# Optimization experiments

Hardware: AMD Instinct MI355X
Metric: run time of the kernel (lower is better)

## Reference

```python
import jax, jax.numpy as jnp
import numpy as np

B, S, MSL, MQL = 512, 20, 32, 16
E, H, HQ = 32, 32, 32
V, A = 10000, 1000
D = H + S  # per-object feature dim (hidden + one-hot tag) = 52
G = 256


def _lstm_last_h(x, Wih, Whh, bih, bhh):
    # x: [N, T, E]; torch LSTM gate order i,f,g,o; returns final hidden [N, H]
    n, t, _ = x.shape
    h_dim = Whh.shape[1]
    xp = jnp.einsum('nte,ge->ntg', x, Wih) + bih + bhh  # precompute input projection

    def step(carry, xt):
        h, c = carry
        gates = xt + h @ Whh.T
        i, f, g, o = jnp.split(gates, 4, axis=-1)
        c = jax.nn.sigmoid(f) * c + jax.nn.sigmoid(i) * jnp.tanh(g)
        h = jax.nn.sigmoid(o) * jnp.tanh(c)
        return (h, c), None

    init = (jnp.zeros((n, h_dim), x.dtype), jnp.zeros((n, h_dim), x.dtype))
    (h, _), _ = jax.lax.scan(step, init, xp.transpose(1, 0, 2))
    return h


def setup_inputs() -> dict:
    key = jax.random.key(0)
    ks = jax.random.split(key, 24)
    nrm = lambda k, shp, std=0.1: (jax.random.normal(k, shp) * std).astype(jnp.float32)
    inp = {
        'story': jax.random.randint(ks[0], (B, S, MSL), 0, V),
        'question': jax.random.randint(ks[1], (B, MQL), 0, V),
        'emb': nrm(ks[2], (V, E)),
        's_Wih': nrm(ks[3], (4 * H, E)),
        's_Whh': nrm(ks[4], (4 * H, H)),
        's_bih': jnp.zeros((4 * H,), jnp.float32),
        's_bhh': jnp.zeros((4 * H,), jnp.float32),
        'q_Wih': nrm(ks[5], (4 * HQ, E)),
        'q_Whh': nrm(ks[6], (4 * HQ, HQ)),
        'q_bih': jnp.zeros((4 * HQ,), jnp.float32),
        'q_bhh': jnp.zeros((4 * HQ,), jnp.float32),
        'g1_w': nrm(ks[7], (G, 2 * D + HQ)), 'g1_b': jnp.zeros((G,), jnp.float32),
        'g2_w': nrm(ks[8], (G, G)), 'g2_b': jnp.zeros((G,), jnp.float32),
        'g3_w': nrm(ks[9], (G, G)), 'g3_b': jnp.zeros((G,), jnp.float32),
        'g4_w': nrm(ks[10], (G, G)), 'g4_b': jnp.zeros((G,), jnp.float32),
        'f1_w': nrm(ks[11], (G, G)), 'f1_b': jnp.zeros((G,), jnp.float32),
        'f2_w': nrm(ks[12], (512, G)), 'f2_b': jnp.zeros((512,), jnp.float32),
        'f3_w': nrm(ks[13], (A, 512)), 'f3_b': jnp.zeros((A,), jnp.float32),
    }
    return inp


def reference(story, question, emb, s_Wih, s_Whh, s_bih, s_bhh,
              q_Wih, q_Whh, q_bih, q_bhh,
              g1_w, g1_b, g2_w, g2_b, g3_w, g3_b, g4_w, g4_b,
              f1_w, f1_b, f2_w, f2_b, f3_w, f3_b):
    bsz = story.shape[0]
    # story encoding: LSTM over each sentence, take final hidden state
    s_emb = emb[story].reshape(bsz * S, MSL, E)
    s_state = _lstm_last_h(s_emb, s_Wih, s_Whh, s_bih, s_bhh).reshape(bsz, S, H)
    # append one-hot position tags -> story objects [B, S, H+S]
    tags = jnp.broadcast_to(jnp.eye(S, dtype=s_state.dtype), (bsz, S, S))
    obj = jnp.concatenate([s_state, tags], axis=2)
    # question encoding
    q_state = _lstm_last_h(emb[question], q_Wih, q_Whh, q_bih, q_bhh)  # [B, HQ]
    # g_theta over all S*S pairs: g1(cat(o_i, o_j, q)) split into three projections
    Wa, Wb, Wq = g1_w[:, :D], g1_w[:, D:2 * D], g1_w[:, 2 * D:]
    pi = jnp.einsum('bsd,gd->bsg', obj, Wa)   # object-as-first projection
    pj = jnp.einsum('bsd,gd->bsg', obj, Wb)   # object-as-second projection
    pq = q_state @ Wq.T                        # [B, G]
    x = jax.nn.relu(pi[:, :, None, :] + pj[:, None, :, :] + pq[:, None, None, :] + g1_b)  # [B,S,S,G]
    x = jax.nn.relu(jnp.einsum('bijg,hg->bijh', x, g2_w) + g2_b)
    x = jax.nn.relu(jnp.einsum('bijg,hg->bijh', x, g3_w) + g3_b)
    x = jax.nn.relu(jnp.einsum('bijg,hg->bijh', x, g4_w) + g4_b)
    sum_g = x.sum(axis=(1, 2))  # [B, G]
    out = jax.nn.relu(sum_g @ f1_w.T + f1_b)
    out = jax.nn.relu(out @ f2_w.T + f2_b)
    return out @ f3_w.T + f3_b
```

## Files before the change

kernel.cpp:

```cpp
#include <hip/hip_runtime.h>

typedef unsigned short u16;
typedef unsigned int   u32;
typedef __attribute__((ext_vector_type(8))) short short8;
typedef __attribute__((ext_vector_type(4))) float f32x4;

#define OFF_XPS   0
#define OFF_XPQ   1280000
#define OFF_QST   2560000
#define OFF_PI    2576384
#define OFF_PJ    5197824
#define OFF_QA    7819264
#define OFF_TGA   7950336
#define OFF_TGB   7955456
#define OFF_WB    7960576
#define OFF_STB   8058880
#define OFF_WAB   8222720
#define OFF_WBB   8226816
#define OFF_WHHS  8230912
#define OFF_WHHQ  8232960
#define OFF_WF1   8235008
#define OFF_WF2   8267776
#define OFF_WF3   8333312
#define OFF_SGP   0
#define OFF_ACT1  720896
#define OFF_ACT2  786432

__device__ __forceinline__ u16 f2bf(float f){
  union { float f; u32 u; } v; v.f = f;
  u32 u = v.u;
  u32 r = u + 0x7fffu + ((u >> 16) & 1u);
  return (u16)(r >> 16);
}
__device__ __forceinline__ u32 pack2(float a, float b){
  u32 r;
  asm("v_cvt_pk_bf16_f32 %0, %1, %2" : "=v"(r) : "v"(a), "v"(b));
  return r;
}
__device__ __forceinline__ float sigm(float x){
  return __builtin_amdgcn_rcpf(1.f + __expf(-x));
}

#define LBAR() do {                                        \
    asm volatile("s_waitcnt lgkmcnt(0)" ::: "memory");     \
    __builtin_amdgcn_s_barrier();                          \
    __builtin_amdgcn_sched_barrier(0);                     \
  } while (0)

__global__ __launch_bounds__(256) void prep_kernel(
    const float* __restrict__ emb,
    const float* __restrict__ swih, const float* __restrict__ sbih, const float* __restrict__ sbhh,
    const float* __restrict__ qwih, const float* __restrict__ qbih, const float* __restrict__ qbhh,
    const float* __restrict__ g2w, const float* __restrict__ g3w, const float* __restrict__ g4w,
    const float* __restrict__ g1w,
    const float* __restrict__ swhh, const float* __restrict__ qwhh,
    const float* __restrict__ f1w, const float* __restrict__ f2w, const float* __restrict__ f3w,
    float* __restrict__ xps, float* __restrict__ xpq,
    u16* __restrict__ wb, u16* __restrict__ wab, u16* __restrict__ wbb,
    float* __restrict__ tga, float* __restrict__ tgb,
    u16* __restrict__ whhbs, u16* __restrict__ whhbq,
    u16* __restrict__ wf1, u16* __restrict__ wf2, u16* __restrict__ wf3)
{
  __shared__ float wl[4096];
  __shared__ float bl[128];
  const int tid = threadIdx.x;
  if (blockIdx.y == 2){
    const int B = 196608;
    const int C = B + 16384;
    const int D = C + 10240;
    const int E = D + 8192;
    const int F = E + 65536;
    const int G = F + 131072;
    const int H = G + 524288;
    for (int idx = blockIdx.x*256 + tid; idx < H; idx += 160*256){
      if (idx < B){
        const int k = idx;
        const float* src = (k < 65536) ? g2w : ((k < 131072) ? g3w : g4w);
        wb[k] = f2bf(src[k & 65535]);
      } else if (idx < C){
        const int k = idx - B;
        if (k < 8192) wab[k] = f2bf(g1w[(k>>5)*136 + (k&31)]);
        else { const int k2 = k - 8192; wbb[k2] = f2bf(g1w[(k2>>5)*136 + 52 + (k2&31)]); }
      } else if (idx < D){
        const int k = idx - C;
        if (k < 5120){ const int s = k >> 8, g = k & 255; tga[k] = g1w[g*136 + 32 + s]; }
        else { const int k2 = k - 5120; const int s = k2 >> 8, g = k2 & 255; tgb[k2] = g1w[g*136 + 84 + s]; }
      } else if (idx < E){
        const int k = idx - D;
        if (k < 4096) whhbs[k] = f2bf(swhh[k]);
        else whhbq[k-4096] = f2bf(qwhh[k-4096]);
      } else if (idx < F){
        const int k = idx - E;
        wf1[k] = f2bf(f1w[k]);
      } else if (idx < G){
        const int k = idx - F;
        wf2[k] = f2bf(f2w[k]);
      } else {
        const int k = idx - G;
        const int o = k >> 9, kk = k & 511;
        wf3[k] = (o < 1000) ? f2bf(f3w[o*512 + kk]) : (u16)0;
      }
    }
    return;
  }
  const bool isq = blockIdx.y;
  const float* wih = isq ? qwih : swih;
  const float* bih = isq ? qbih : sbih;
  const float* bhh = isq ? qbhh : sbhh;
  float* xp = isq ? xpq : xps;
  #pragma unroll
  for (int k=0;k<16;k++) wl[k*256+tid] = wih[k*256+tid];
  if (tid < 128) bl[tid] = bih[tid] + bhh[tid];
  __syncthreads();
  const int v = blockIdx.x*256 + tid;
  if (v >= 10000) return;
  float4 e[8];
  #pragma unroll
  for (int q=0;q<8;q++) e[q] = *(const float4*)(emb + v*32 + q*4);
  for (int g=0; g<128; ++g){
    float acc = bl[g];
    #pragma unroll
    for (int q=0;q<8;q++){
      float4 w4 = *(const float4*)(&wl[g*32 + q*4]);
      acc = fmaf(e[q].x, w4.x, acc); acc = fmaf(e[q].y, w4.y, acc);
      acc = fmaf(e[q].z, w4.z, acc); acc = fmaf(e[q].w, w4.w, acc);
    }
    xp[v*128 + (g&15)*8 + (g>>4)] = acc;
  }
}

template<int LEN>
__device__ __forceinline__ void lstm_mfma_run(
    const int* __restrict__ toks, int s0,
    const float* __restrict__ xpr, const u16* __restrict__ whhb,
    u16* __restrict__ hl, int lane, float* h0r, float* h1r)
{
  const int l15 = lane & 15, l4 = lane >> 4;
  short8 wf[8];
  #pragma unroll
  for (int f=0; f<8; f++)
    wf[f] = *(const short8*)(whhb + (f*16+l15)*32 + l4*8);
  short8 ha = (short8){0,0,0,0,0,0,0,0};
  float c0[4] = {0,0,0,0}, c1[4] = {0,0,0,0};
  int tk[4];
  #pragma unroll
  for (int r=0;r<4;r++) tk[r] = toks[(s0 + l4*4 + r)*LEN];
  float4 xa[4], xb[4];
  #pragma unroll
  for (int r=0;r<4;r++){
    xa[r] = *(const float4*)(xpr + tk[r]*128 + l15*8);
    xb[r] = *(const float4*)(xpr + tk[r]*128 + l15*8 + 4);
  }
  #pragma unroll
  for (int t=0; t<LEN; ++t){
    int tkn[4];
    if (t+1 < LEN){
      #pragma unroll
      for (int r=0;r<4;r++) tkn[r] = toks[(s0 + l4*4 + r)*LEN + t + 1];
    }
    const f32x4 z = (f32x4){0.f,0.f,0.f,0.f};
    f32x4 acc[8];
    #pragma unroll
    for (int f=0; f<8; f++)
      acc[f] = __builtin_amdgcn_mfma_f32_16x16x32_bf16(ha, wf[f], z, 0, 0, 0);
    float4 na[4], nb[4];
    if (t+1 < LEN){
      #pragma unroll
      for (int r=0;r<4;r++){
        na[r] = *(const float4*)(xpr + tkn[r]*128 + l15*8);
        nb[r] = *(const float4*)(xpr + tkn[r]*128 + l15*8 + 4);
      }
    }
    #pragma unroll
    for (int r=0;r<4;r++){
      float i0 = sigm(acc[0][r] + xa[r].x);
      float f0 = sigm(acc[2][r] + xa[r].z);
      float g0 = 2.f*sigm(2.f*(acc[4][r] + xb[r].x)) - 1.f;
      float o0 = sigm(acc[6][r] + xb[r].z);
      c0[r] = fmaf(f0, c0[r], i0*g0);
      h0r[r] = o0 * (2.f*sigm(2.f*c0[r]) - 1.f);
      float i1 = sigm(acc[1][r] + xa[r].y);
      float f1v = sigm(acc[3][r] + xa[r].w);
      float g1v = 2.f*sigm(2.f*(acc[5][r] + xb[r].y)) - 1.f;
      float o1 = sigm(acc[7][r] + xb[r].w);
      c1[r] = fmaf(f1v, c1[r], i1*g1v);
      h1r[r] = o1 * (2.f*sigm(2.f*c1[r]) - 1.f);
    }
    if (t+1 < LEN){
      #pragma unroll
      for (int r=0;r<4;r++){
        hl[(l4*4+r)*32 + l15]      = f2bf(h0r[r]);
        hl[(l4*4+r)*32 + 16 + l15] = f2bf(h1r[r]);
      }
      __syncthreads();
      ha = *(const short8*)(hl + l15*32 + l4*8);
      #pragma unroll
      for (int r=0;r<4;r++){ xa[r] = na[r]; xb[r] = nb[r]; }
    }
  }
}

__global__ __launch_bounds__(64) void lstm_kernel(
    const int* __restrict__ story, const int* __restrict__ question,
    const float* __restrict__ xprs, const float* __restrict__ xprq,
    const u16* __restrict__ whhbs, const u16* __restrict__ whhbq,
    u16* __restrict__ stb, float* __restrict__ qst)
{
  __shared__ u16 hl[512];
  const int lane = threadIdx.x;
  const int w = blockIdx.x;
  const int l15 = lane & 15, l4 = lane >> 4;
  float h0r[4], h1r[4];
  if (w >= 640){
    const int s0 = (w - 640)*16;
    lstm_mfma_run<16>(question, s0, xprq, whhbq, hl, lane, h0r, h1r);
    #pragma unroll
    for (int r=0;r<4;r++){
      qst[(s0 + l4*4 + r)*32 + l15]      = h0r[r];
      qst[(s0 + l4*4 + r)*32 + 16 + l15] = h1r[r];
    }
  } else {
    const int s0 = w*16;
    lstm_mfma_run<32>(story, s0, xprs, whhbs, hl, lane, h0r, h1r);
    #pragma unroll
    for (int r=0;r<4;r++){
      stb[(s0 + l4*4 + r)*32 + l15]      = f2bf(h0r[r]);
      stb[(s0 + l4*4 + r)*32 + 16 + l15] = f2bf(h1r[r]);
    }
  }
}

__global__ __launch_bounds__(256) void pipj_kernel(
    const u16* __restrict__ stb, const u16* __restrict__ wab, const u16* __restrict__ wbb,
    const float* __restrict__ tga, const float* __restrict__ tgb,
    const float* __restrict__ qst, const float* __restrict__ g1w, const float* __restrict__ g1b,
    float* __restrict__ pi, float* __restrict__ pj, float* __restrict__ qa)
{
  const int tid = threadIdx.x;
  if (blockIdx.y == 2){
    for (int idx = blockIdx.x*256 + tid; idx < 131072; idx += 160*256){
      const int b = idx >> 8, g = idx & 255;
      const float* qs = qst + b*32;
      const float* wr = g1w + g*136 + 104;
      float acc = g1b[g];
      #pragma unroll
      for (int q=0;q<8;q++){
        float4 s4 = *(const float4*)(qs + q*4);
        float4 w4 = *(const float4*)(wr + q*4);
        acc = fmaf(s4.x, w4.x, acc); acc = fmaf(s4.y, w4.y, acc);
        acc = fmaf(s4.z, w4.z, acc); acc = fmaf(s4.w, w4.w, acc);
      }
      qa[idx] = acc;
    }
    return;
  }
  const int lane = tid & 63;
  const int wv = tid >> 6;
  const int l15 = lane & 15;
  const int l4r = lane >> 4;
  const int bs0 = blockIdx.x * 64;
  const bool isj = blockIdx.y;
  const u16* wB = isj ? wbb : wab;
  const float* tg = isj ? tgb : tga;
  float* out = isj ? pj : pi;

  short8 af[4], bf[4];
  #pragma unroll
  for (int mf=0; mf<4; mf++)
    af[mf] = *(const short8*)(stb + (bs0 + mf*16 + l15)*32 + l4r*8);
  #pragma unroll
  for (int nf=0; nf<4; nf++)
    bf[nf] = *(const short8*)(wB + (wv*64 + nf*16 + l15)*32 + l4r*8);

  #pragma unroll
  for (int mf=0; mf<4; mf++){
    #pragma unroll
    for (int nf=0; nf<4; nf++){
      f32x4 acc = (f32x4){0.f,0.f,0.f,0.f};
      acc = __builtin_amdgcn_mfma_f32_16x16x32_bf16(af[mf], bf[nf], acc, 0, 0, 0);
      const int g = wv*64 + nf*16 + l15;
      #pragma unroll
      for (int r=0; r<4; r++){
        const int bs = bs0 + mf*16 + l4r*4 + r;
        const int s = bs % 20;
        out[bs*256 + g] = acc[r] + tg[s*256 + g];
      }
    }
  }
}

#define LDX 264
__global__ __launch_bounds__(512) void relnet_kernel(
    const float* __restrict__ pi, const float* __restrict__ pj, const float* __restrict__ qa,
    const u16* __restrict__ w2, const u16* __restrict__ w3, const u16* __restrict__ w4,
    const float* __restrict__ b2, const float* __restrict__ b3, const float* __restrict__ b4,
    float* __restrict__ sgp)
{
  __shared__ u16 Xs[80*LDX + 6656];
  const int tid = threadIdx.x;
  const int lane = tid & 63;
  const int wv  = tid >> 6;
  const int b   = blockIdx.x;
  const int t   = blockIdx.y;
  const int l15 = lane & 15;
  const int l4  = lane >> 4;

  const float* pib = pi + b*(20*256);
  const float* pjb = pj + b*(20*256);
  const float* qab = qa + b*256;

  const int ar0 = (wv*32 + l15)*256 + l4*8;
  const int ar1 = (wv*32 + 16 + l15)*256 + l4*8;

  #pragma unroll
  for (int it = 0; it < 5; ++it){
    int u  = it*512 + tid;
    int m  = u >> 5;
    int gq = (u & 31) << 3;
    int R  = t*80 + m;
    int i  = R / 20;
    int j  = R - i*20;
    const float4* pr = (const float4*)(pib + i*256 + gq);
    const float4* qr = (const float4*)(pjb + j*256 + gq);
    const float4* ar = (const float4*)(qab + gq);
    uint4 pk;
    {
      float4 a = pr[0], c4 = qr[0], d4 = ar[0];
      pk.x = pack2(fmaxf(a.x+c4.x+d4.x,0.f), fmaxf(a.y+c4.y+d4.y,0.f));
      pk.y = pack2(fmaxf(a.z+c4.z+d4.z,0.f), fmaxf(a.w+c4.w+d4.w,0.f));
    }
    {
      float4 a = pr[1], c4 = qr[1], d4 = ar[1];
      pk.z = pack2(fmaxf(a.x+c4.x+d4.x,0.f), fmaxf(a.y+c4.y+d4.y,0.f));
      pk.w = pack2(fmaxf(a.z+c4.z+d4.z,0.f), fmaxf(a.w+c4.w+d4.w,0.f));
    }
    *(uint4*)(&Xs[m*LDX + gq]) = pk;
  }

  short8 pf0 = *(const short8*)(w2 + ar0);
  short8 pf1 = *(const short8*)(w2 + ar1);

  LBAR();

  #pragma unroll
  for (int lay = 0; lay < 2; ++lay){
    const u16*   W    = lay ? w3 : w2;
    const u16*   Wn   = lay ? w4 : w3;
    const float* bias = lay ? b3 : b2;
    f32x4 acc[2][5];
    #pragma unroll
    for (int hf=0; hf<2; hf++)
      #pragma unroll
      for (int mf=0; mf<5; mf++)
        acc[hf][mf] = (f32x4){0.f,0.f,0.f,0.f};

    #pragma unroll
    for (int kk = 0; kk < 8; ++kk){
      short8 a0 = pf0, a1 = pf1;
      const u16* src = (kk < 7) ? W : Wn;
      const int  kn  = (kk < 7) ? (kk+1)*32 : 0;
      pf0 = *(const short8*)(src + ar0 + kn);
      pf1 = *(const short8*)(src + ar1 + kn);
      short8 xf[5];
      #pragma unroll
      for (int mf=0; mf<5; mf++)
        xf[mf] = *(const short8*)(&Xs[(mf*16 + l15)*LDX + kk*32 + l4*8]);
      #pragma unroll
      for (int mf=0; mf<5; mf++){
        acc[0][mf] = __builtin_amdgcn_mfma_f32_16x16x32_bf16(a0, xf[mf], acc[0][mf], 0, 0, 0);
        acc[1][mf] = __builtin_amdgcn_mfma_f32_16x16x32_bf16(a1, xf[mf], acc[1][mf], 0, 0, 0);
      }
    }

    LBAR();
    #pragma unroll
    for (int hf=0; hf<2; hf++){
      int h0 = wv*32 + hf*16 + l4*4;
      float4 bi = *(const float4*)(bias + h0);
      #pragma unroll
      for (int mf=0; mf<5; mf++){
        int m = mf*16 + l15;
        uint2 pk;
        pk.x = pack2(fmaxf(acc[hf][mf][0]+bi.x,0.f), fmaxf(acc[hf][mf][1]+bi.y,0.f));
        pk.y = pack2(fmaxf(acc[hf][mf][2]+bi.z,0.f), fmaxf(acc[hf][mf][3]+bi.w,0.f));
        *(uint2*)(&Xs[m*LDX + h0]) = pk;
      }
    }
    LBAR();
  }

  {
    f32x4 acc[2][5];
    #pragma unroll
    for (int hf=0; hf<2; hf++)
      #pragma unroll
      for (int mf=0; mf<5; mf++)
        acc[hf][mf] = (f32x4){0.f,0.f,0.f,0.f};

    #pragma unroll
    for (int kk = 0; kk < 8; ++kk){
      short8 a0 = pf0, a1 = pf1;
      if (kk < 7){
        pf0 = *(const short8*)(w4 + ar0 + (kk+1)*32);
        pf1 = *(const short8*)(w4 + ar1 + (kk+1)*32);
      }
      short8 xf[5];
      #pragma unroll
      for (int mf=0; mf<5; mf++)
        xf[mf] = *(const short8*)(&Xs[(mf*16 + l15)*LDX + kk*32 + l4*8]);
      #pragma unroll
      for (int mf=0; mf<5; mf++){
        acc[0][mf] = __builtin_amdgcn_mfma_f32_16x16x32_bf16(a0, xf[mf], acc[0][mf], 0, 0, 0);
        acc[1][mf] = __builtin_amdgcn_mfma_f32_16x16x32_bf16(a1, xf[mf], acc[1][mf], 0, 0, 0);
      }
    }

    #pragma unroll
    for (int hf=0; hf<2; hf++){
      int h0 = wv*32 + hf*16 + l4*4;
      float4 bi = *(const float4*)(b4 + h0);
      float s0 = 0.f, s1 = 0.f, s2 = 0.f, s3 = 0.f;
      #pragma unroll
      for (int mf=0; mf<5; mf++){
        s0 += fmaxf(acc[hf][mf][0]+bi.x,0.f);
        s1 += fmaxf(acc[hf][mf][1]+bi.y,0.f);
        s2 += fmaxf(acc[hf][mf][2]+bi.z,0.f);
        s3 += fmaxf(acc[hf][mf][3]+bi.w,0.f);
      }
      float sv[4] = {s0, s1, s2, s3};
      #pragma unroll
      for (int r=0; r<4; r++){
        float v = sv[r];
        v += __shfl_xor(v, 1);
        v += __shfl_xor(v, 2);
        v += __shfl_xor(v, 4);
        v += __shfl_xor(v, 8);
        if (l15 == 0){
          int h = h0 + r;
          sgp[t*131072 + b*256 + h] = v;
        }
      }
    }
  }
}

__global__ __launch_bounds__(256) void fcm1_kernel(
    const float* __restrict__ sgp, const u16* __restrict__ w,
    const float* __restrict__ bias, u16* __restrict__ outp)
{
  const int tid = threadIdx.x, lane = tid & 63, wv = tid >> 6;
  const int l15 = lane & 15, l4 = lane >> 4;
  const int b0 = blockIdx.x*16;
  const int of0 = blockIdx.y*4 + wv;
  f32x4 acc = (f32x4){0.f,0.f,0.f,0.f};
  #pragma unroll
  for (int kk=0; kk<8; ++kk){
    const float* base = sgp + (b0+l15)*256 + kk*32 + l4*8;
    float4 s0 = {0.f,0.f,0.f,0.f}, s1 = {0.f,0.f,0.f,0.f};
    #pragma unroll
    for (int t=0;t<5;t++){
      float4 a = *(const float4*)(base + t*131072);
      float4 c = *(const float4*)(base + t*131072 + 4);
      s0.x += a.x; s0.y += a.y; s0.z += a.z; s0.w += a.w;
      s1.x += c.x; s1.y += c.y; s1.z += c.z; s1.w += c.w;
    }
    union { short8 s; u32 u[4]; } xf;
    xf.u[0] = pack2(s0.x, s0.y); xf.u[1] = pack2(s0.z, s0.w);
    xf.u[2] = pack2(s1.x, s1.y); xf.u[3] = pack2(s1.z, s1.w);
    short8 af = *(const short8*)(w + (of0*16 + l15)*256 + kk*32 + l4*8);
    acc = __builtin_amdgcn_mfma_f32_16x16x32_bf16(af, xf.s, acc, 0, 0, 0);
  }
  const int b = b0 + l15;
  const int o0 = of0*16 + l4*4;
  float v0 = fmaxf(acc[0] + bias[o0+0], 0.f);
  float v1 = fmaxf(acc[1] + bias[o0+1], 0.f);
  float v2 = fmaxf(acc[2] + bias[o0+2], 0.f);
  float v3 = fmaxf(acc[3] + bias[o0+3], 0.f);
  uint2 pk;
  pk.x = pack2(v0, v1);
  pk.y = pack2(v2, v3);
  *(uint2*)(outp + (size_t)b*256 + o0) = pk;
}

template<int HF, int KK, int OPAD, int OREAL, int MODE>
__global__ __launch_bounds__(256) void fcm_kernel(
    const u16* __restrict__ in, const u16* __restrict__ w,
    const float* __restrict__ bias, void* __restrict__ outp)
{
  const int K = KK*32;
  const int tid = threadIdx.x, lane = tid & 63, wv = tid >> 6;
  const int l15 = lane & 15, l4 = lane >> 4;
  const int b0 = blockIdx.x*16;
  const int of0 = (blockIdx.y*4 + wv)*HF;
  f32x4 acc[HF];
  #pragma unroll
  for (int hf=0; hf<HF; hf++) acc[hf] = (f32x4){0.f,0.f,0.f,0.f};
  #pragma unroll 4
  for (int kk=0; kk<KK; ++kk){
    short8 xf = *(const short8*)(in + (b0+l15)*K + kk*32 + l4*8);
    #pragma unroll
    for (int hf=0; hf<HF; hf++){
      short8 af = *(const short8*)(w + ((of0+hf)*16 + l15)*K + kk*32 + l4*8);
      acc[hf] = __builtin_amdgcn_mfma_f32_16x16x32_bf16(af, xf, acc[hf], 0, 0, 0);
    }
  }
  const int b = b0 + l15;
  #pragma unroll
  for (int hf=0; hf<HF; hf++){
    const int o0 = (of0+hf)*16 + l4*4;
    float v[4];
    #pragma unroll
    for (int r=0;r<4;r++){
      float bv = (o0+r < OREAL) ? bias[o0+r] : 0.f;
      v[r] = acc[hf][r] + bv;
    }
    if (MODE == 0){
      uint2 pk;
      pk.x = pack2(fmaxf(v[0],0.f), fmaxf(v[1],0.f));
      pk.y = pack2(fmaxf(v[2],0.f), fmaxf(v[3],0.f));
      *(uint2*)((u16*)outp + (size_t)b*OPAD + o0) = pk;
    } else {
      float* of = (float*)outp;
      #pragma unroll
      for (int r=0;r<4;r++)
        if (o0+r < OREAL) of[(size_t)b*OREAL + o0 + r] = v[r];
    }
  }
}

extern "C" void kernel_launch(void* const* d_in, const int* in_sizes, int n_in,
                              void* d_out, int out_size, void* d_ws, size_t ws_size,
                              hipStream_t stream)
{
  const int*   story    = (const int*)d_in[0];
  const int*   question = (const int*)d_in[1];
  const float* emb   = (const float*)d_in[2];
  const float* s_wih = (const float*)d_in[3];
  const float* s_whh = (const float*)d_in[4];
  const float* s_bih = (const float*)d_in[5];
  const float* s_bhh = (const float*)d_in[6];
  const float* q_wih = (const float*)d_in[7];
  const float* q_whh = (const float*)d_in[8];
  const float* q_bih = (const float*)d_in[9];
  const float* q_bhh = (const float*)d_in[10];
  const float* g1w = (const float*)d_in[11];
  const float* g1b = (const float*)d_in[12];
  const float* g2w = (const float*)d_in[13];
  const float* g2b = (const float*)d_in[14];
  const float* g3w = (const float*)d_in[15];
  const float* g3b = (const float*)d_in[16];
  const float* g4w = (const float*)d_in[17];
  const float* g4b = (const float*)d_in[18];
  const float* f1w = (const float*)d_in[19];
  const float* f1b = (const float*)d_in[20];
  const float* f2w = (const float*)d_in[21];
  const float* f2b = (const float*)d_in[22];
  const float* f3w = (const float*)d_in[23];
  const float* f3b = (const float*)d_in[24];

  float* ws  = (float*)d_ws;
  float* xps = ws + OFF_XPS;
  float* xpq = ws + OFF_XPQ;
  float* qst = ws + OFF_QST;
  float* pi  = ws + OFF_PI;
  float* pj  = ws + OFF_PJ;
  float* qa  = ws + OFF_QA;
  float* tga = ws + OFF_TGA;
  float* tgb = ws + OFF_TGB;
  float* sgp = ws + OFF_SGP;
  u16*   wb    = (u16*)(ws + OFF_WB);
  u16*   w2b   = wb;
  u16*   w3b   = wb + 65536;
  u16*   w4b   = wb + 131072;
  u16*   stb   = (u16*)(ws + OFF_STB);
  u16*   wab   = (u16*)(ws + OFF_WAB);
  u16*   wbb   = (u16*)(ws + OFF_WBB);
  u16*   whhbs = (u16*)(ws + OFF_WHHS);
  u16*   whhbq = (u16*)(ws + OFF_WHHQ);
  u16*   wf1   = (u16*)(ws + OFF_WF1);
  u16*   wf2   = (u16*)(ws + OFF_WF2);
  u16*   wf3   = (u16*)(ws + OFF_WF3);
  u16*   act1  = (u16*)(ws + OFF_ACT1);
  u16*   act2  = (u16*)(ws + OFF_ACT2);

  prep_kernel<<<dim3(160,3), dim3(256), 0, stream>>>(
      emb, s_wih, s_bih, s_bhh, q_wih, q_bih, q_bhh,
      g2w, g3w, g4w, g1w, s_whh, q_whh, f1w, f2w, f3w,
      xps, xpq, wb, wab, wbb, tga, tgb, whhbs, whhbq, wf1, wf2, wf3);
  lstm_kernel<<<dim3(672), dim3(64), 0, stream>>>(
      story, question, xps, xpq, whhbs, whhbq, stb, qst);
  pipj_kernel<<<dim3(160,3), dim3(256), 0, stream>>>(
      stb, wab, wbb, tga, tgb, qst, g1w, g1b, pi, pj, qa);
  relnet_kernel<<<dim3(512,5), dim3(512), 0, stream>>>(
      pi, pj, qa, w2b, w3b, w4b, g2b, g3b, g4b, sgp);
  fcm1_kernel<<<dim3(32,4), dim3(256), 0, stream>>>(sgp, wf1, f1b, act1);
  fcm_kernel<2,8,512,512,0><<<dim3(32,4), dim3(256), 0, stream>>>(act1, wf2, f2b, act2);
  fcm_kernel<2,16,1024,1000,1><<<dim3(32,8), dim3(256), 0, stream>>>(act2, wf3, f3b, (float*)d_out);
}
```

Before: 236.0 us.

## Split prep projection across gate halves and double-buffer LDS operand loads

The prep kernel's LSTM input projection now gives each block half of the 128 gates, which halves per-block LDS weight storage and the per-thread loop length while doubling the number of active blocks. In the g2–g4 MFMA loops, the LDS activation fragments for the next k-step are loaded before the current MFMAs issue (register double-buffering). The MFMA bursts are wrapped in s_setprio so the wave gets higher scheduling priority during them. This aims to hide LDS latency behind matrix math and add parallelism in prep, at the cost of more VGPRs, which could lower occupancy.

```diff
diff --git a/kernel.cpp b/kernel.cpp
--- a/kernel.cpp
+++ b/kernel.cpp
@@ -61,8 +61,8 @@
     u16* __restrict__ whhbs, u16* __restrict__ whhbq,
     u16* __restrict__ wf1, u16* __restrict__ wf2, u16* __restrict__ wf3)
 {
-  __shared__ float wl[4096];
-  __shared__ float bl[128];
+  __shared__ float wl[2048];
+  __shared__ float bl[64];
   const int tid = threadIdx.x;
   if (blockIdx.y == 2){
     const int B = 196608;
@@ -103,25 +103,28 @@
     }
     return;
   }
+  if (blockIdx.x >= 80) return;
   const bool isq = blockIdx.y;
   const float* wih = isq ? qwih : swih;
   const float* bih = isq ? qbih : sbih;
   const float* bhh = isq ? qbhh : sbhh;
   float* xp = isq ? xpq : xps;
-  #pragma unroll
-  for (int k=0;k<16;k++) wl[k*256+tid] = wih[k*256+tid];
-  if (tid < 128) bl[tid] = bih[tid] + bhh[tid];
+  const int gh = (blockIdx.x & 1) * 64;
+  #pragma unroll
+  for (int k=0;k<8;k++) wl[k*256+tid] = wih[gh*32 + k*256 + tid];
+  if (tid < 64) bl[tid] = bih[gh+tid] + bhh[gh+tid];
   __syncthreads();
-  const int v = blockIdx.x*256 + tid;
+  const int v = (blockIdx.x >> 1)*256 + tid;
   if (v >= 10000) return;
   float4 e[8];
   #pragma unroll
   for (int q=0;q<8;q++) e[q] = *(const float4*)(emb + v*32 + q*4);
-  for (int g=0; g<128; ++g){
-    float acc = bl[g];
+  for (int g2=0; g2<64; ++g2){
+    const int g = gh + g2;
+    float acc = bl[g2];
     #pragma unroll
     for (int q=0;q<8;q++){
-      float4 w4 = *(const float4*)(&wl[g*32 + q*4]);
+      float4 w4 = *(const float4*)(&wl[g2*32 + q*4]);
       acc = fmaf(e[q].x, w4.x, acc); acc = fmaf(e[q].y, w4.y, acc);
       acc = fmaf(e[q].z, w4.z, acc); acc = fmaf(e[q].w, w4.w, acc);
     }
@@ -354,6 +357,11 @@
       for (int mf=0; mf<5; mf++)
         acc[hf][mf] = (f32x4){0.f,0.f,0.f,0.f};
 
+    short8 xc[5];
+    #pragma unroll
+    for (int mf=0; mf<5; mf++)
+      xc[mf] = *(const short8*)(&Xs[(mf*16 + l15)*LDX + l4*8]);
+
     #pragma unroll
     for (int kk = 0; kk < 8; ++kk){
       short8 a0 = pf0, a1 = pf1;
@@ -361,14 +369,22 @@
       const int  kn  = (kk < 7) ? (kk+1)*32 : 0;
       pf0 = *(const short8*)(src + ar0 + kn);
       pf1 = *(const short8*)(src + ar1 + kn);
-      short8 xf[5];
-      #pragma unroll
-      for (int mf=0; mf<5; mf++)
-        xf[mf] = *(const short8*)(&Xs[(mf*16 + l15)*LDX + kk*32 + l4*8]);
+      short8 xn[5];
+      if (kk < 7){
+        #pragma unroll
+        for (int mf=0; mf<5; mf++)
+          xn[mf] = *(const short8*)(&Xs[(mf*16 + l15)*LDX + (kk+1)*32 + l4*8]);
+      }
+      __builtin_amdgcn_s_setprio(1);
       #pragma unroll
       for (int mf=0; mf<5; mf++){
-        acc[0][mf] = __builtin_amdgcn_mfma_f32_16x16x32_bf16(a0, xf[mf], acc[0][mf], 0, 0, 0);
-        acc[1][mf] = __builtin_amdgcn_mfma_f32_16x16x32_bf16(a1, xf[mf], acc[1][mf], 0, 0, 0);
+        acc[0][mf] = __builtin_amdgcn_mfma_f32_16x16x32_bf16(a0, xc[mf], acc[0][mf], 0, 0, 0);
+        acc[1][mf] = __builtin_amdgcn_mfma_f32_16x16x32_bf16(a1, xc[mf], acc[1][mf], 0, 0, 0);
+      }
+      __builtin_amdgcn_s_setprio(0);
+      if (kk < 7){
+        #pragma unroll
+        for (int mf=0; mf<5; mf++) xc[mf] = xn[mf];
       }
     }
 
@@ -397,6 +413,11 @@
       for (int mf=0; mf<5; mf++)
         acc[hf][mf] = (f32x4){0.f,0.f,0.f,0.f};
 
+    short8 xc[5];
+    #pragma unroll
+    for (int mf=0; mf<5; mf++)
+      xc[mf] = *(const short8*)(&Xs[(mf*16 + l15)*LDX + l4*8]);
+
     #pragma unroll
     for (int kk = 0; kk < 8; ++kk){
       short8 a0 = pf0, a1 = pf1;
@@ -404,14 +425,22 @@
         pf0 = *(const short8*)(w4 + ar0 + (kk+1)*32);
         pf1 = *(const short8*)(w4 + ar1 + (kk+1)*32);
       }
-      short8 xf[5];
-      #pragma unroll
-      for (int mf=0; mf<5; mf++)
-        xf[mf] = *(const short8*)(&Xs[(mf*16 + l15)*LDX + kk*32 + l4*8]);
+      short8 xn[5];
+      if (kk < 7){
+        #pragma unroll
+        for (int mf=0; mf<5; mf++)
+          xn[mf] = *(const short8*)(&Xs[(mf*16 + l15)*LDX + (kk+1)*32 + l4*8]);
+      }
+      __builtin_amdgcn_s_setprio(1);
       #pragma unroll
       for (int mf=0; mf<5; mf++){
-        acc[0][mf] = __builtin_amdgcn_mfma_f32_16x16x32_bf16(a0, xf[mf], acc[0][mf], 0, 0, 0);
-        acc[1][mf] = __builtin_amdgcn_mfma_f32_16x16x32_bf16(a1, xf[mf], acc[1][mf], 0, 0, 0);
+        acc[0][mf] = __builtin_amdgcn_mfma_f32_16x16x32_bf16(a0, xc[mf], acc[0][mf], 0, 0, 0);
+        acc[1][mf] = __builtin_amdgcn_mfma_f32_16x16x32_bf16(a1, xc[mf], acc[1][mf], 0, 0, 0);
+      }
+      __builtin_amdgcn_s_setprio(0);
+      if (kk < 7){
+        #pragma unroll
+        for (int mf=0; mf<5; mf++) xc[mf] = xn[mf];
       }
     }
 
```

New measurement: 231.6 us. No clear change (-1.9%).
